# Performance work log

Measured on AMD Instinct MI355X. Metric: run time of the kernel, lower is better.

The kernel has to match this reference:

```python
import jax, jax.numpy as jnp
import numpy as np

N = 50000       # nodes
E = 1200000     # edges (before self-loops)
IN_CH = 128
HID = 64
L = 3           # FAConv layers
EPS_RES = 0.1   # FAConv eps residual weight
BN_EPS = 1e-5


def _bn(x, g, b):
    # BatchNorm1d, training-mode statistics (biased variance, like torch)
    mu = x.mean(axis=0)
    var = x.var(axis=0)
    return g * (x - mu) * jax.lax.rsqrt(var + BN_EPS) + b


def setup_inputs() -> dict:
    key = jax.random.key(0)
    ks = jax.random.split(key, 12)
    s = lambda d: 1.0 / np.sqrt(d)
    H2 = HID // 2
    return {
        "x": jax.random.normal(ks[0], (N, IN_CH), jnp.float32),
        "edge_index": jax.random.randint(ks[1], (2, E), 0, N, dtype=jnp.int32),
        "batch_size": 10000,
        "W_in": jax.random.normal(ks[2], (IN_CH, HID), jnp.float32) * s(IN_CH),
        "b_in": jnp.zeros((HID,), jnp.float32),
        "att_l": jax.random.normal(ks[3], (L, HID), jnp.float32) * s(HID),
        "att_r": jax.random.normal(ks[4], (L, HID), jnp.float32) * s(HID),
        "bn_g": jnp.ones((L, HID), jnp.float32),
        "bn_b": jnp.zeros((L, HID), jnp.float32),
        "W1": jax.random.normal(ks[5], (HID, HID), jnp.float32) * s(HID),
        "b1": jnp.zeros((HID,), jnp.float32),
        "g1": jnp.ones((HID,), jnp.float32),
        "be1": jnp.zeros((HID,), jnp.float32),
        "W2": jax.random.normal(ks[6], (HID, H2), jnp.float32) * s(HID),
        "b2": jnp.zeros((H2,), jnp.float32),
        "g2": jnp.ones((H2,), jnp.float32),
        "be2": jnp.zeros((H2,), jnp.float32),
        "W3": jax.random.normal(ks[7], (H2, 1), jnp.float32) * s(H2),
        "b3": jnp.zeros((1,), jnp.float32),
    }


def reference(x, edge_index, batch_size, W_in, b_in, att_l, att_r, bn_g, bn_b,
              W1, b1, g1, be1, W2, b2, g2, be2, W3, b3):
    n = x.shape[0]
    # gcn_norm with self-loops (same for all layers since graph is fixed)
    loops = jnp.arange(n, dtype=edge_index.dtype)
    src = jnp.concatenate([edge_index[0], loops])  # j (source)
    dst = jnp.concatenate([edge_index[1], loops])  # i (target)
    deg = jax.ops.segment_sum(jnp.ones_like(dst, dtype=x.dtype), dst, num_segments=n)
    dinv = jnp.where(deg > 0, jax.lax.rsqrt(deg), 0.0)
    norm = dinv[src] * dinv[dst]                   # [E+N]

    x0 = jax.nn.relu(x @ W_in + b_in)              # [N, HID]
    h = x0
    for l in range(L):
        al = h @ att_l[l]                          # [N] att_l^T x
        ar = h @ att_r[l]                          # [N] att_r^T x
        alpha = jnp.tanh(al[src] + ar[dst])        # [E+N] signed attention
        msg = h[src] * (alpha * norm)[:, None]     # gather + weight
        out = jax.ops.segment_sum(msg, dst, num_segments=n) + EPS_RES * x0
        h = _bn(jax.nn.relu(out), bn_g[l], bn_b[l])

    z = h[:batch_size]
    z = jax.nn.relu(_bn(z @ W1 + b1, g1, be1))
    z = jax.nn.relu(_bn(z @ W2 + b2, g2, be2))
    return (z @ W3 + b3).squeeze(-1)
```

## Files before the change

kernel.cpp:

```cpp
#include <hip/hip_runtime.h>
#include <hip/hip_bf16.h>
#include <math.h>

#define NND 50000
#define NE  1200000
#define TOT (NE + NND)
#define INCH 128
#define HID 64
#define H2  32
#define NL  3
#define BSZ 10000
#define NB  196
#define NHB 128
#define NSTAT 256
#define CHUNK 4096
#define EPS_RES 0.1f
#define BN_EPS 1e-5f

typedef unsigned short ushort8v __attribute__((ext_vector_type(8)));

__device__ __forceinline__ float b2f(unsigned short u) {
    return __uint_as_float((unsigned)u << 16);
}

__device__ __forceinline__ float fast_tanh(float x) {
    float cx = fminf(fmaxf(x, -8.f), 8.f);
    float e = __expf(2.f * cx);
    return 1.f - __fdividef(2.f, e + 1.f);
}


__global__ __launch_bounds__(256) void bhist_kernel(const int* __restrict__ dst, int* __restrict__ bh_part, int ne) {
    __shared__ int arr[256];
    arr[threadIdx.x] = 0;
    __syncthreads();
    int i = blockIdx.x * 256 + threadIdx.x;
    int stride = gridDim.x * 256;
    for (int e = i; e < ne; e += stride) atomicAdd(&arr[dst[e] >> 8], 1);
    __syncthreads();
    bh_part[blockIdx.x * 256 + threadIdx.x] = arr[threadIdx.x];
}

__global__ __launch_bounds__(256) void bscan_kernel(const int* __restrict__ bh_part,
                                                    int* __restrict__ bstart, int* __restrict__ bcur,
                                                    int* __restrict__ offsets) {
    __shared__ int ls[256];
    int t = threadIdx.x;
    int v = 0;
    for (int k = 0; k < NHB; k++) v += bh_part[k * 256 + t];
    ls[t] = v;
    __syncthreads();
    for (int off = 1; off < 256; off <<= 1) {
        int tv = (t >= off) ? ls[t - off] : 0;
        __syncthreads();
        ls[t] += tv;
        __syncthreads();
    }
    int excl = ls[t] - v;
    if (t < NB) { bstart[t] = excl; bcur[t] = excl; }
    if (t == NB) bstart[NB] = ls[NB - 1];
    if (t == 0) offsets[NND] = TOT;
}

__global__ __launch_bounds__(256) void passA_kernel(const int* __restrict__ src, const int* __restrict__ dst,
                                                    int* __restrict__ bcur, unsigned* __restrict__ ebuf, int ne) {
    __shared__ int arr[256];
    int t = threadIdx.x;
    int base = blockIdx.x * CHUNK;
    int lim = min(base + CHUNK, ne);
    arr[t] = 0;
    __syncthreads();
    for (int e = base + t; e < lim; e += 256) atomicAdd(&arr[dst[e] >> 8], 1);
    __syncthreads();
    int cnt_t = arr[t];
    int claimed = 0;
    if (cnt_t > 0) claimed = atomicAdd(&bcur[t], cnt_t);
    __syncthreads();
    arr[t] = claimed;
    __syncthreads();
    for (int e = base + t; e < lim; e += 256) {
        int d = dst[e];
        int pos = atomicAdd(&arr[d >> 8], 1);
        ebuf[pos] = ((unsigned)src[e] << 8) | (unsigned)(d & 255);
    }
}

__global__ __launch_bounds__(256) void bucket_build_kernel(const unsigned* __restrict__ ebuf, const int* __restrict__ bstart,
                                                           int* __restrict__ offsets, int* __restrict__ csr,
                                                           float* __restrict__ aldi_f) {
    __shared__ int dcnt[256];
    __shared__ int ls[256];
    __shared__ int cur[256];
    int b = blockIdx.x, t = threadIdx.x;
    dcnt[t] = 0;
    __syncthreads();
    int beg = bstart[b], end = bstart[b + 1];
    for (int p = beg + t; p < end; p += 256) atomicAdd(&dcnt[ebuf[p] & 255u], 1);
    __syncthreads();
    int node = b * 256 + t;
    bool valid = node < NND;
    int d = valid ? (dcnt[t] + 1) : 0;
    ls[t] = d;
    __syncthreads();
    for (int off = 1; off < 256; off <<= 1) {
        int tv = (t >= off) ? ls[t - off] : 0;
        __syncthreads();
        ls[t] += tv;
        __syncthreads();
    }
    int off = bstart[b] + b * 256 + ls[t] - d;
    if (valid) {
        offsets[node] = off;
        aldi_f[2 * node + 1] = rsqrtf((float)d);
        csr[off] = node;
        cur[t] = off + 1;
    }
    __syncthreads();
    for (int p = beg + t; p < end; p += 256) {
        unsigned ed = ebuf[p];
        int pos = atomicAdd(&cur[ed & 255u], 1);
        csr[pos] = (int)(ed >> 8);
    }
}

__global__ __launch_bounds__(256) void gemm_in_kernel(const float* __restrict__ x, const float* __restrict__ W,
                                                      const float* __restrict__ b,
                                                      const float* __restrict__ attl, const float* __restrict__ attr,
                                                      __hip_bfloat16* __restrict__ x0bf,
                                                      float* __restrict__ aldi_f, float* __restrict__ ar) {
    __shared__ float Wl[INCH * HID];
    __shared__ float xs[16 * INCH];
    int t = threadIdx.x;
    for (int i = t; i < INCH * HID; i += 256) Wl[i] = W[i];
    size_t rowbase = (size_t)blockIdx.x * 16;
    for (int i = t; i < 16 * INCH; i += 256) xs[i] = x[rowbase * INCH + i];
    __syncthreads();
    int col = t & 63, rg = t >> 6;
    float a0 = 0.f, a1 = 0.f, a2 = 0.f, a3 = 0.f;
    for (int k = 0; k < INCH; k++) {
        float wk = Wl[k * HID + col];
        a0 = fmaf(xs[(rg * 4 + 0) * INCH + k], wk, a0);
        a1 = fmaf(xs[(rg * 4 + 1) * INCH + k], wk, a1);
        a2 = fmaf(xs[(rg * 4 + 2) * INCH + k], wk, a2);
        a3 = fmaf(xs[(rg * 4 + 3) * INCH + k], wk, a3);
    }
    float bb = b[col];
    a0 = fmaxf(a0 + bb, 0.f); a1 = fmaxf(a1 + bb, 0.f);
    a2 = fmaxf(a2 + bb, 0.f); a3 = fmaxf(a3 + bb, 0.f);
    size_t r = rowbase + rg * 4;
    x0bf[(r + 0) * HID + col] = __float2bfloat16(a0);
    x0bf[(r + 1) * HID + col] = __float2bfloat16(a1);
    x0bf[(r + 2) * HID + col] = __float2bfloat16(a2);
    x0bf[(r + 3) * HID + col] = __float2bfloat16(a3);
    float wl = attl[col], wr = attr[col];
    float p0 = a0 * wl, q0 = a0 * wr, p1 = a1 * wl, q1 = a1 * wr;
    float p2 = a2 * wl, q2 = a2 * wr, p3 = a3 * wl, q3 = a3 * wr;
    for (int off = 32; off > 0; off >>= 1) {
        p0 += __shfl_xor(p0, off); q0 += __shfl_xor(q0, off);
        p1 += __shfl_xor(p1, off); q1 += __shfl_xor(q1, off);
        p2 += __shfl_xor(p2, off); q2 += __shfl_xor(q2, off);
        p3 += __shfl_xor(p3, off); q3 += __shfl_xor(q3, off);
    }
    if (col == 0) {
        aldi_f[2 * (r + 0)] = p0; ar[r + 0] = q0;
        aldi_f[2 * (r + 1)] = p1; ar[r + 1] = q1;
        aldi_f[2 * (r + 2)] = p2; ar[r + 2] = q2;
        aldi_f[2 * (r + 3)] = p3; ar[r + 3] = q3;
    }
}

__global__ __launch_bounds__(256) void aggregate_kernel(const __hip_bfloat16* __restrict__ hbf,
                                                        const __hip_bfloat16* __restrict__ x0bf,
                                                        const float2* __restrict__ aldi,
                                                        const float* __restrict__ ar,
                                                        const int* __restrict__ offsets, const int* __restrict__ csr,
                                                        float* __restrict__ y, int n) {
    int v = (blockIdx.x * 256 + threadIdx.x) >> 6;
    int lane = threadIdx.x & 63;
    if (v >= n) return;
    int g = lane >> 3;
    int cl = (lane & 7) << 3;
    int beg = offsets[v], end = offsets[v + 1];
    float arv = ar[v];
    const unsigned short* hb = (const unsigned short*)hbf;
    float a0 = 0.f, a1 = 0.f, a2 = 0.f, a3 = 0.f, a4 = 0.f, a5 = 0.f, a6 = 0.f, a7 = 0.f;
    for (int base = beg; base < end; base += 64) {
        int p = base + lane;
        int u = 0; float c = 0.f;
        if (p < end) {
            u = csr[p];
            float2 ad = aldi[u];
            c = fast_tanh(ad.x + arv) * ad.y;
        }
        int cnt = min(64, end - base);
        int iters = (cnt + 7) >> 3;
        int j = g;
        int js = (j < cnt) ? j : 0;
        int uj = __shfl(u, js);
        float cj = __shfl(c, js);
        if (j >= cnt) cj = 0.f;
        ushort8v hv = *(const ushort8v*)(hb + (size_t)uj * HID + cl);
        for (int it = 1; it < iters; ++it) {
            int jn = (it << 3) + g;
            int jsn = (jn < cnt) ? jn : 0;
            int ujn = __shfl(u, jsn);
            float cjn = __shfl(c, jsn);
            if (jn >= cnt) cjn = 0.f;
            ushort8v hvn = *(const ushort8v*)(hb + (size_t)ujn * HID + cl);
            a0 = fmaf(b2f(hv[0]), cj, a0);
            a1 = fmaf(b2f(hv[1]), cj, a1);
            a2 = fmaf(b2f(hv[2]), cj, a2);
            a3 = fmaf(b2f(hv[3]), cj, a3);
            a4 = fmaf(b2f(hv[4]), cj, a4);
            a5 = fmaf(b2f(hv[5]), cj, a5);
            a6 = fmaf(b2f(hv[6]), cj, a6);
            a7 = fmaf(b2f(hv[7]), cj, a7);
            hv = hvn; cj = cjn;
        }
        a0 = fmaf(b2f(hv[0]), cj, a0);
        a1 = fmaf(b2f(hv[1]), cj, a1);
        a2 = fmaf(b2f(hv[2]), cj, a2);
        a3 = fmaf(b2f(hv[3]), cj, a3);
        a4 = fmaf(b2f(hv[4]), cj, a4);
        a5 = fmaf(b2f(hv[5]), cj, a5);
        a6 = fmaf(b2f(hv[6]), cj, a6);
        a7 = fmaf(b2f(hv[7]), cj, a7);
    }
    for (int off = 8; off < 64; off <<= 1) {
        a0 += __shfl_xor(a0, off); a1 += __shfl_xor(a1, off);
        a2 += __shfl_xor(a2, off); a3 += __shfl_xor(a3, off);
        a4 += __shfl_xor(a4, off); a5 += __shfl_xor(a5, off);
        a6 += __shfl_xor(a6, off); a7 += __shfl_xor(a7, off);
    }
    if (g == 0) {
        float dv = aldi[v].y;
        ushort8v xb = *(const ushort8v*)((const unsigned short*)x0bf + (size_t)v * HID + cl);
        float4 o0, o1;
        o0.x = fmaxf(fmaf(EPS_RES, b2f(xb[0]), a0 * dv), 0.f);
        o0.y = fmaxf(fmaf(EPS_RES, b2f(xb[1]), a1 * dv), 0.f);
        o0.z = fmaxf(fmaf(EPS_RES, b2f(xb[2]), a2 * dv), 0.f);
        o0.w = fmaxf(fmaf(EPS_RES, b2f(xb[3]), a3 * dv), 0.f);
        o1.x = fmaxf(fmaf(EPS_RES, b2f(xb[4]), a4 * dv), 0.f);
        o1.y = fmaxf(fmaf(EPS_RES, b2f(xb[5]), a5 * dv), 0.f);
        o1.z = fmaxf(fmaf(EPS_RES, b2f(xb[6]), a6 * dv), 0.f);
        o1.w = fmaxf(fmaf(EPS_RES, b2f(xb[7]), a7 * dv), 0.f);
        *(float4*)(y + (size_t)v * HID + cl) = o0;
        *(float4*)(y + (size_t)v * HID + cl + 4) = o1;
    }
}

template <int C>
__global__ __launch_bounds__(256) void bn_stats_fused_kernel(const float* __restrict__ y, int rows,
                                                             const float* __restrict__ g, const float* __restrict__ b,
                                                             float rows_inv,
                                                             float* __restrict__ acc, int* __restrict__ counter,
                                                             float* __restrict__ scale, float* __restrict__ shift) {
    const int TPR = C / 4;
    const int RPW = 64 / TPR;
    int lane = threadIdx.x & 63;
    int wave = threadIdx.x >> 6;
    int cl = (lane % TPR) * 4;
    int rsub = lane / TPR;
    int rpb = 4 * RPW;
    int r = blockIdx.x * rpb + wave * RPW + rsub;
    int stride = gridDim.x * rpb;
    float s0 = 0.f, s1 = 0.f, s2 = 0.f, s3 = 0.f, q0 = 0.f, q1 = 0.f, q2 = 0.f, q3 = 0.f;
    for (; r < rows; r += stride) {
        float4 v = *(const float4*)(y + (size_t)r * C + cl);
        s0 += v.x; q0 = fmaf(v.x, v.x, q0);
        s1 += v.y; q1 = fmaf(v.y, v.y, q1);
        s2 += v.z; q2 = fmaf(v.z, v.z, q2);
        s3 += v.w; q3 = fmaf(v.w, v.w, q3);
    }
    for (int off = TPR; off < 64; off <<= 1) {
        s0 += __shfl_xor(s0, off); q0 += __shfl_xor(q0, off);
        s1 += __shfl_xor(s1, off); q1 += __shfl_xor(q1, off);
        s2 += __shfl_xor(s2, off); q2 += __shfl_xor(q2, off);
        s3 += __shfl_xor(s3, off); q3 += __shfl_xor(q3, off);
    }
    __shared__ float lsum[4][64], lsq[4][64];
    if (lane < TPR) {
        lsum[wave][cl + 0] = s0; lsq[wave][cl + 0] = q0;
        lsum[wave][cl + 1] = s1; lsq[wave][cl + 1] = q1;
        lsum[wave][cl + 2] = s2; lsq[wave][cl + 2] = q2;
        lsum[wave][cl + 3] = s3; lsq[wave][cl + 3] = q3;
    }
    __syncthreads();
    int t = threadIdx.x;
    if (t < C) {
        float ts = lsum[0][t] + lsum[1][t] + lsum[2][t] + lsum[3][t];
        float tq = lsq[0][t] + lsq[1][t] + lsq[2][t] + lsq[3][t];
        atomicAdd(&acc[t], ts);
        atomicAdd(&acc[64 + t], tq);
    }
    __shared__ int islast;
    __syncthreads();
    if (t == 0) {
        __threadfence();
        int old = atomicAdd(counter, 1);
        islast = (old == (int)gridDim.x - 1) ? 1 : 0;
    }
    __syncthreads();
    if (islast && t < C) {
        float ts = atomicAdd(&acc[t], 0.f);
        float tq = atomicAdd(&acc[64 + t], 0.f);
        float mean = ts * rows_inv;
        float var = tq * rows_inv - mean * mean;
        float sc = g[t] * rsqrtf(var + BN_EPS);
        scale[t] = sc;
        shift[t] = b[t] - mean * sc;
        atomicExch(&acc[t], 0.f);
        atomicExch(&acc[64 + t], 0.f);
        if (t == 0) atomicExch(counter, 0);
    }
}

__global__ __launch_bounds__(256) void bnapply_attn_kernel(const float* __restrict__ y, const float* __restrict__ scale,
                                                           const float* __restrict__ shift,
                                                           const float* __restrict__ attl, const float* __restrict__ attr,
                                                           __hip_bfloat16* __restrict__ hbf,
                                                           float* __restrict__ aldi_f, float* __restrict__ ar, int n) {
    int v = (blockIdx.x * 256 + threadIdx.x) >> 6;
    int lane = threadIdx.x & 63;
    if (v >= n) return;
    float val = fmaf(y[(size_t)v * HID + lane], scale[lane], shift[lane]);
    hbf[(size_t)v * HID + lane] = __float2bfloat16(val);
    float pl = val * attl[lane];
    float pr = val * attr[lane];
    for (int off = 32; off > 0; off >>= 1) {
        pl += __shfl_xor(pl, off);
        pr += __shfl_xor(pr, off);
    }
    if (lane == 0) { aldi_f[2 * v] = pl; ar[v] = pr; }
}

__global__ __launch_bounds__(256) void mlp1_kernel(const float* __restrict__ y, const float* __restrict__ scale,
                                                   const float* __restrict__ shift, const float* __restrict__ W,
                                                   const float* __restrict__ b, float* __restrict__ z1) {
    __shared__ float Wl[HID * HID];
    __shared__ float xs[16 * HID];
    int t = threadIdx.x;
    for (int i = t; i < HID * HID; i += 256) Wl[i] = W[i];
    size_t rowbase = (size_t)blockIdx.x * 16;
    for (int i = t; i < 16 * HID; i += 256) {
        int c = i & 63;
        xs[i] = fmaf(y[rowbase * HID + i], scale[c], shift[c]);
    }
    __syncthreads();
    int col = t & 63, rg = t >> 6;
    float a0 = 0.f, a1 = 0.f, a2 = 0.f, a3 = 0.f;
    for (int k = 0; k < HID; k++) {
        float wk = Wl[k * HID + col];
        a0 = fmaf(xs[(rg * 4 + 0) * HID + k], wk, a0);
        a1 = fmaf(xs[(rg * 4 + 1) * HID + k], wk, a1);
        a2 = fmaf(xs[(rg * 4 + 2) * HID + k], wk, a2);
        a3 = fmaf(xs[(rg * 4 + 3) * HID + k], wk, a3);
    }
    float bb = b[col];
    size_t r = rowbase + rg * 4;
    z1[(r + 0) * HID + col] = a0 + bb;
    z1[(r + 1) * HID + col] = a1 + bb;
    z1[(r + 2) * HID + col] = a2 + bb;
    z1[(r + 3) * HID + col] = a3 + bb;
}

__global__ __launch_bounds__(256) void mlp2_kernel(const float* __restrict__ z1, const float* __restrict__ scale,
                                                   const float* __restrict__ shift, const float* __restrict__ W,
                                                   const float* __restrict__ b, float* __restrict__ z2) {
    __shared__ float Wl[HID * H2];
    __shared__ float as[16 * HID];
    int t = threadIdx.x;
    for (int i = t; i < HID * H2; i += 256) Wl[i] = W[i];
    size_t rowbase = (size_t)blockIdx.x * 16;
    for (int i = t; i < 16 * HID; i += 256) {
        int c = i & 63;
        float v = z1[rowbase * HID + i];
        as[i] = fmaxf(fmaf(v, scale[c], shift[c]), 0.f);
    }
    __syncthreads();
    int col = t & 31, rg = t >> 5;
    float a0 = 0.f, a1 = 0.f;
    for (int k = 0; k < HID; k++) {
        float wk = Wl[k * H2 + col];
        a0 = fmaf(as[(rg * 2 + 0) * HID + k], wk, a0);
        a1 = fmaf(as[(rg * 2 + 1) * HID + k], wk, a1);
    }
    float bb = b[col];
    size_t r = rowbase + rg * 2;
    z2[(r + 0) * H2 + col] = a0 + bb;
    z2[(r + 1) * H2 + col] = a1 + bb;
}

__global__ __launch_bounds__(256) void mlp3_kernel(const float* __restrict__ z2, const float* __restrict__ scale,
                                                   const float* __restrict__ shift, const float* __restrict__ W3,
                                                   const float* __restrict__ b3, float* __restrict__ out, int rows) {
    int i = blockIdx.x * 256 + threadIdx.x;
    if (i >= rows) return;
    float acc = 0.f;
#pragma unroll
    for (int k = 0; k < H2; k++) {
        float v = fmaxf(fmaf(z2[(size_t)i * H2 + k], scale[k], shift[k]), 0.f);
        acc = fmaf(v, W3[k], acc);
    }
    out[i] = acc + b3[0];
}

extern "C" void kernel_launch(void* const* d_in, const int* in_sizes, int n_in,
                              void* d_out, int out_size, void* d_ws, size_t ws_size,
                              hipStream_t stream) {
    const float* x     = (const float*)d_in[0];
    const int*   ei    = (const int*)d_in[1];
    const int*   src   = ei;
    const int*   dst   = ei + NE;
    const float* W_in  = (const float*)d_in[3];
    const float* b_in  = (const float*)d_in[4];
    const float* att_l = (const float*)d_in[5];
    const float* att_r = (const float*)d_in[6];
    const float* bn_g  = (const float*)d_in[7];
    const float* bn_b  = (const float*)d_in[8];
    const float* W1    = (const float*)d_in[9];
    const float* b1    = (const float*)d_in[10];
    const float* g1    = (const float*)d_in[11];
    const float* be1   = (const float*)d_in[12];
    const float* W2    = (const float*)d_in[13];
    const float* b2    = (const float*)d_in[14];
    const float* g2    = (const float*)d_in[15];
    const float* be2   = (const float*)d_in[16];
    const float* W3    = (const float*)d_in[17];
    const float* b3    = (const float*)d_in[18];
    float* out = (float*)d_out;

    char* p = (char*)d_ws;
    auto carve = [&](size_t bytes) -> void* {
        void* r = (void*)p;
        p += (bytes + 255) & ~(size_t)255;
        return r;
    };
    int*   bh_part = (int*)carve((size_t)NHB * 256 * 4);
    int*   bstart  = (int*)carve(256 * 4);
    int*   bcur    = (int*)carve(256 * 4);
    int*   offsets = (int*)carve((size_t)(NND + 1) * 4);
    int*   csr     = (int*)carve((size_t)TOT * 4);
    float2* aldi   = (float2*)carve((size_t)NND * 8);
    float* ar      = (float*)carve((size_t)NND * 4);
    __hip_bfloat16* x0bf = (__hip_bfloat16*)carve((size_t)NND * HID * 2);
    __hip_bfloat16* hbfA = (__hip_bfloat16*)carve((size_t)NND * HID * 2);
    __hip_bfloat16* hbfB = (__hip_bfloat16*)carve((size_t)NND * HID * 2);
    float* ybuf    = (float*)carve((size_t)NND * HID * 4);
    unsigned* ebuf = (unsigned*)ybuf;
    float* acc     = (float*)carve(132 * 4);
    int*   counter = (int*)(acc + 128);
    float* scale   = (float*)carve(64 * 4);
    float* shift   = (float*)carve(64 * 4);
    float* z1      = (float*)carve((size_t)BSZ * HID * 4);
    float* z2      = (float*)carve((size_t)BSZ * H2 * 4);

    const int nblkA = (NE + CHUNK - 1) / CHUNK;

    hipMemsetAsync(acc, 0, 132 * 4, stream);

    bhist_kernel<<<NHB, 256, 0, stream>>>(dst, bh_part, NE);
    gemm_in_kernel<<<NND / 16, 256, 0, stream>>>(x, W_in, b_in, att_l, att_r, x0bf, (float*)aldi, ar);
    bscan_kernel<<<1, 256, 0, stream>>>(bh_part, bstart, bcur, offsets);
    passA_kernel<<<nblkA, 256, 0, stream>>>(src, dst, bcur, ebuf, NE);
    bucket_build_kernel<<<NB, 256, 0, stream>>>(ebuf, bstart, offsets, csr, (float*)aldi);

    const __hip_bfloat16* h_in = x0bf;
    __hip_bfloat16* hbufs[2] = {hbfA, hbfB};
    for (int l = 0; l < NL; l++) {
        aggregate_kernel<<<NND / 4, 256, 0, stream>>>(h_in, x0bf, aldi, ar, offsets, csr, ybuf, NND);
        bn_stats_fused_kernel<64><<<NSTAT, 256, 0, stream>>>(ybuf, NND, bn_g + l * HID, bn_b + l * HID,
                                                             1.0f / NND, acc, counter, scale, shift);
        if (l < NL - 1) {
            bnapply_attn_kernel<<<NND / 4, 256, 0, stream>>>(ybuf, scale, shift,
                                                             att_l + (l + 1) * HID, att_r + (l + 1) * HID,
                                                             hbufs[l], (float*)aldi, ar, NND);
            h_in = hbufs[l];
        }
    }

    mlp1_kernel<<<BSZ / 16, 256, 0, stream>>>(ybuf, scale, shift, W1, b1, z1);
    bn_stats_fused_kernel<64><<<NSTAT, 256, 0, stream>>>(z1, BSZ, g1, be1, 1.0f / BSZ, acc, counter, scale, shift);

    mlp2_kernel<<<BSZ / 16, 256, 0, stream>>>(z1, scale, shift, W2, b2, z2);
    bn_stats_fused_kernel<32><<<NSTAT, 256, 0, stream>>>(z2, BSZ, g2, be2, 1.0f / BSZ, acc, counter, scale, shift);

    mlp3_kernel<<<(BSZ + 255) / 256, 256, 0, stream>>>(z2, scale, shift, W3, b3, out, BSZ);
}
```

Measured before the change: 364.5 us.

## Fuse BN stats with apply via grid barrier; unroll aggregate gather by four

Merges the BatchNorm statistics kernel and the BN-apply/attention kernel for the first two layers into one persistent kernel that spins on a global counter as a grid-wide barrier. This saves a launch and keeps part of the feature buffer warm in cache. The aggregate loop is also restructured to issue four independent neighbour row loads per iteration instead of a one-deep software prefetch, to get more memory parallelism. Each BN use now gets its own zeroed accumulator slot instead of resetting shared ones, which relies on all 256 blocks being co-resident for the spin barrier.

```diff
diff --git a/kernel.cpp b/kernel.cpp
--- a/kernel.cpp
+++ b/kernel.cpp
@@ -193,38 +193,39 @@
             c = fast_tanh(ad.x + arv) * ad.y;
         }
         int cnt = min(64, end - base);
-        int iters = (cnt + 7) >> 3;
-        int j = g;
-        int js = (j < cnt) ? j : 0;
-        int uj = __shfl(u, js);
-        float cj = __shfl(c, js);
-        if (j >= cnt) cj = 0.f;
-        ushort8v hv = *(const ushort8v*)(hb + (size_t)uj * HID + cl);
-        for (int it = 1; it < iters; ++it) {
-            int jn = (it << 3) + g;
-            int jsn = (jn < cnt) ? jn : 0;
-            int ujn = __shfl(u, jsn);
-            float cjn = __shfl(c, jsn);
-            if (jn >= cnt) cjn = 0.f;
-            ushort8v hvn = *(const ushort8v*)(hb + (size_t)ujn * HID + cl);
-            a0 = fmaf(b2f(hv[0]), cj, a0);
-            a1 = fmaf(b2f(hv[1]), cj, a1);
-            a2 = fmaf(b2f(hv[2]), cj, a2);
-            a3 = fmaf(b2f(hv[3]), cj, a3);
-            a4 = fmaf(b2f(hv[4]), cj, a4);
-            a5 = fmaf(b2f(hv[5]), cj, a5);
-            a6 = fmaf(b2f(hv[6]), cj, a6);
-            a7 = fmaf(b2f(hv[7]), cj, a7);
-            hv = hvn; cj = cjn;
+        int nchunk = (cnt + 31) >> 5;
+        for (int ch = 0; ch < nchunk; ++ch) {
+            int j0 = (ch << 5) + g;
+            int j1 = j0 + 8, j2 = j0 + 16, j3 = j0 + 24;
+            int js0 = (j0 < cnt) ? j0 : 0;
+            int js1 = (j1 < cnt) ? j1 : 0;
+            int js2 = (j2 < cnt) ? j2 : 0;
+            int js3 = (j3 < cnt) ? j3 : 0;
+            int u0 = __shfl(u, js0); float c0 = __shfl(c, js0); if (j0 >= cnt) c0 = 0.f;
+            int u1 = __shfl(u, js1); float c1 = __shfl(c, js1); if (j1 >= cnt) c1 = 0.f;
+            int u2 = __shfl(u, js2); float c2 = __shfl(c, js2); if (j2 >= cnt) c2 = 0.f;
+            int u3 = __shfl(u, js3); float c3 = __shfl(c, js3); if (j3 >= cnt) c3 = 0.f;
+            ushort8v h0 = *(const ushort8v*)(hb + (size_t)u0 * HID + cl);
+            ushort8v h1 = *(const ushort8v*)(hb + (size_t)u1 * HID + cl);
+            ushort8v h2 = *(const ushort8v*)(hb + (size_t)u2 * HID + cl);
+            ushort8v h3 = *(const ushort8v*)(hb + (size_t)u3 * HID + cl);
+            a0 = fmaf(b2f(h0[0]), c0, a0); a1 = fmaf(b2f(h0[1]), c0, a1);
+            a2 = fmaf(b2f(h0[2]), c0, a2); a3 = fmaf(b2f(h0[3]), c0, a3);
+            a4 = fmaf(b2f(h0[4]), c0, a4); a5 = fmaf(b2f(h0[5]), c0, a5);
+            a6 = fmaf(b2f(h0[6]), c0, a6); a7 = fmaf(b2f(h0[7]), c0, a7);
+            a0 = fmaf(b2f(h1[0]), c1, a0); a1 = fmaf(b2f(h1[1]), c1, a1);
+            a2 = fmaf(b2f(h1[2]), c1, a2); a3 = fmaf(b2f(h1[3]), c1, a3);
+            a4 = fmaf(b2f(h1[4]), c1, a4); a5 = fmaf(b2f(h1[5]), c1, a5);
+            a6 = fmaf(b2f(h1[6]), c1, a6); a7 = fmaf(b2f(h1[7]), c1, a7);
+            a0 = fmaf(b2f(h2[0]), c2, a0); a1 = fmaf(b2f(h2[1]), c2, a1);
+            a2 = fmaf(b2f(h2[2]), c2, a2); a3 = fmaf(b2f(h2[3]), c2, a3);
+            a4 = fmaf(b2f(h2[4]), c2, a4); a5 = fmaf(b2f(h2[5]), c2, a5);
+            a6 = fmaf(b2f(h2[6]), c2, a6); a7 = fmaf(b2f(h2[7]), c2, a7);
+            a0 = fmaf(b2f(h3[0]), c3, a0); a1 = fmaf(b2f(h3[1]), c3, a1);
+            a2 = fmaf(b2f(h3[2]), c3, a2); a3 = fmaf(b2f(h3[3]), c3, a3);
+            a4 = fmaf(b2f(h3[4]), c3, a4); a5 = fmaf(b2f(h3[5]), c3, a5);
+            a6 = fmaf(b2f(h3[6]), c3, a6); a7 = fmaf(b2f(h3[7]), c3, a7);
         }
-        a0 = fmaf(b2f(hv[0]), cj, a0);
-        a1 = fmaf(b2f(hv[1]), cj, a1);
-        a2 = fmaf(b2f(hv[2]), cj, a2);
-        a3 = fmaf(b2f(hv[3]), cj, a3);
-        a4 = fmaf(b2f(hv[4]), cj, a4);
-        a5 = fmaf(b2f(hv[5]), cj, a5);
-        a6 = fmaf(b2f(hv[6]), cj, a6);
-        a7 = fmaf(b2f(hv[7]), cj, a7);
     }
     for (int off = 8; off < 64; off <<= 1) {
         a0 += __shfl_xor(a0, off); a1 += __shfl_xor(a1, off);
@@ -309,29 +310,90 @@
         float sc = g[t] * rsqrtf(var + BN_EPS);
         scale[t] = sc;
         shift[t] = b[t] - mean * sc;
-        atomicExch(&acc[t], 0.f);
-        atomicExch(&acc[64 + t], 0.f);
-        if (t == 0) atomicExch(counter, 0);
-    }
-}
-
-__global__ __launch_bounds__(256) void bnapply_attn_kernel(const float* __restrict__ y, const float* __restrict__ scale,
-                                                           const float* __restrict__ shift,
-                                                           const float* __restrict__ attl, const float* __restrict__ attr,
-                                                           __hip_bfloat16* __restrict__ hbf,
-                                                           float* __restrict__ aldi_f, float* __restrict__ ar, int n) {
-    int v = (blockIdx.x * 256 + threadIdx.x) >> 6;
+    }
+}
+
+__global__ __launch_bounds__(256) void bn_fused_apply_attn_kernel(const float* __restrict__ y, int rows,
+                                                                  const float* __restrict__ g, const float* __restrict__ b,
+                                                                  float rows_inv,
+                                                                  float* __restrict__ acc, int* __restrict__ counter,
+                                                                  const float* __restrict__ attl, const float* __restrict__ attr,
+                                                                  __hip_bfloat16* __restrict__ hbf,
+                                                                  float* __restrict__ aldi_f, float* __restrict__ ar) {
+    const int TPR = 16;
     int lane = threadIdx.x & 63;
-    if (v >= n) return;
-    float val = fmaf(y[(size_t)v * HID + lane], scale[lane], shift[lane]);
-    hbf[(size_t)v * HID + lane] = __float2bfloat16(val);
-    float pl = val * attl[lane];
-    float pr = val * attr[lane];
-    for (int off = 32; off > 0; off >>= 1) {
-        pl += __shfl_xor(pl, off);
-        pr += __shfl_xor(pr, off);
-    }
-    if (lane == 0) { aldi_f[2 * v] = pl; ar[v] = pr; }
+    int wave = threadIdx.x >> 6;
+    int cl = (lane % TPR) * 4;
+    int rsub = lane / TPR;
+    int r = blockIdx.x * 16 + wave * 4 + rsub;
+    int stride = gridDim.x * 16;
+    float s0 = 0.f, s1 = 0.f, s2 = 0.f, s3 = 0.f, q0 = 0.f, q1 = 0.f, q2 = 0.f, q3 = 0.f;
+    for (; r < rows; r += stride) {
+        float4 v = *(const float4*)(y + (size_t)r * HID + cl);
+        s0 += v.x; q0 = fmaf(v.x, v.x, q0);
+        s1 += v.y; q1 = fmaf(v.y, v.y, q1);
+        s2 += v.z; q2 = fmaf(v.z, v.z, q2);
+        s3 += v.w; q3 = fmaf(v.w, v.w, q3);
+    }
+    for (int off = TPR; off < 64; off <<= 1) {
+        s0 += __shfl_xor(s0, off); q0 += __shfl_xor(q0, off);
+        s1 += __shfl_xor(s1, off); q1 += __shfl_xor(q1, off);
+        s2 += __shfl_xor(s2, off); q2 += __shfl_xor(q2, off);
+        s3 += __shfl_xor(s3, off); q3 += __shfl_xor(q3, off);
+    }
+    __shared__ float lsum[4][64], lsq[4][64];
+    if (lane < TPR) {
+        lsum[wave][cl + 0] = s0; lsq[wave][cl + 0] = q0;
+        lsum[wave][cl + 1] = s1; lsq[wave][cl + 1] = q1;
+        lsum[wave][cl + 2] = s2; lsq[wave][cl + 2] = q2;
+        lsum[wave][cl + 3] = s3; lsq[wave][cl + 3] = q3;
+    }
+    __syncthreads();
+    int t = threadIdx.x;
+    if (t < 64) {
+        float ts = lsum[0][t] + lsum[1][t] + lsum[2][t] + lsum[3][t];
+        float tq = lsq[0][t] + lsq[1][t] + lsq[2][t] + lsq[3][t];
+        atomicAdd(&acc[t], ts);
+        atomicAdd(&acc[64 + t], tq);
+    }
+    __syncthreads();
+    if (t == 0) {
+        __threadfence();
+        atomicAdd(counter, 1);
+        while (atomicAdd(counter, 0) < (int)gridDim.x) {
+            __builtin_amdgcn_s_sleep(2);
+        }
+    }
+    __syncthreads();
+    __shared__ float s_scale[64], s_shift[64];
+    if (t < 64) {
+        float ts = atomicAdd(&acc[t], 0.f);
+        float tq = atomicAdd(&acc[64 + t], 0.f);
+        float mean = ts * rows_inv;
+        float var = tq * rows_inv - mean * mean;
+        float sc = g[t] * rsqrtf(var + BN_EPS);
+        s_scale[t] = sc;
+        s_shift[t] = b[t] - mean * sc;
+    }
+    __syncthreads();
+    float scl = s_scale[lane], shf = s_shift[lane];
+    float wl = attl[lane], wr = attr[lane];
+    for (int r0 = blockIdx.x * 16 + wave * 4; r0 < rows; r0 += stride) {
+#pragma unroll
+        for (int i = 0; i < 4; i++) {
+            int rr = r0 + i;
+            if (rr >= rows) break;
+            float val = fmaf(y[(size_t)rr * HID + lane], scl, shf);
+            hbf[(size_t)rr * HID + lane] = __float2bfloat16(val);
+            float pl = val * wl;
+            float pr = val * wr;
+            for (int off = 32; off > 0; off >>= 1) {
+                pl += __shfl_xor(pl, off);
+                pr += __shfl_xor(pr, off);
+            }
+            if (lane == 0) { aldi_f[2 * rr] = pl; ar[rr] = pr; }
+        }
+    }
 }
 
 __global__ __launch_bounds__(256) void mlp1_kernel(const float* __restrict__ y, const float* __restrict__ scale,
@@ -448,16 +510,18 @@
     __hip_bfloat16* hbfB = (__hip_bfloat16*)carve((size_t)NND * HID * 2);
     float* ybuf    = (float*)carve((size_t)NND * HID * 4);
     unsigned* ebuf = (unsigned*)ybuf;
-    float* acc     = (float*)carve(132 * 4);
-    int*   counter = (int*)(acc + 128);
+    float* accall  = (float*)carve(5 * 256 * 4);
     float* scale   = (float*)carve(64 * 4);
     float* shift   = (float*)carve(64 * 4);
     float* z1      = (float*)carve((size_t)BSZ * HID * 4);
     float* z2      = (float*)carve((size_t)BSZ * H2 * 4);
 
+    auto accr = [&](int i) -> float* { return accall + i * 256; };
+    auto ctr  = [&](int i) -> int*   { return (int*)(accall + i * 256 + 128); };
+
     const int nblkA = (NE + CHUNK - 1) / CHUNK;
 
-    hipMemsetAsync(acc, 0, 132 * 4, stream);
+    hipMemsetAsync(accall, 0, 5 * 256 * 4, stream);
 
     bhist_kernel<<<NHB, 256, 0, stream>>>(dst, bh_part, NE);
     gemm_in_kernel<<<NND / 16, 256, 0, stream>>>(x, W_in, b_in, att_l, att_r, x0bf, (float*)aldi, ar);
@@ -469,21 +533,23 @@
     __hip_bfloat16* hbufs[2] = {hbfA, hbfB};
     for (int l = 0; l < NL; l++) {
         aggregate_kernel<<<NND / 4, 256, 0, stream>>>(h_in, x0bf, aldi, ar, offsets, csr, ybuf, NND);
-        bn_stats_fused_kernel<64><<<NSTAT, 256, 0, stream>>>(ybuf, NND, bn_g + l * HID, bn_b + l * HID,
-                                                             1.0f / NND, acc, counter, scale, shift);
         if (l < NL - 1) {
-            bnapply_attn_kernel<<<NND / 4, 256, 0, stream>>>(ybuf, scale, shift,
-                                                             att_l + (l + 1) * HID, att_r + (l + 1) * HID,
-                                                             hbufs[l], (float*)aldi, ar, NND);
+            bn_fused_apply_attn_kernel<<<NSTAT, 256, 0, stream>>>(ybuf, NND, bn_g + l * HID, bn_b + l * HID,
+                                                                  1.0f / NND, accr(l), ctr(l),
+                                                                  att_l + (l + 1) * HID, att_r + (l + 1) * HID,
+                                                                  hbufs[l], (float*)aldi, ar);
             h_in = hbufs[l];
+        } else {
+            bn_stats_fused_kernel<64><<<NSTAT, 256, 0, stream>>>(ybuf, NND, bn_g + l * HID, bn_b + l * HID,
+                                                                 1.0f / NND, accr(2), ctr(2), scale, shift);
         }
     }
 
     mlp1_kernel<<<BSZ / 16, 256, 0, stream>>>(ybuf, scale, shift, W1, b1, z1);
-    bn_stats_fused_kernel<64><<<NSTAT, 256, 0, stream>>>(z1, BSZ, g1, be1, 1.0f / BSZ, acc, counter, scale, shift);
+    bn_stats_fused_kernel<64><<<NSTAT, 256, 0, stream>>>(z1, BSZ, g1, be1, 1.0f / BSZ, accr(3), ctr(3), scale, shift);
 
     mlp2_kernel<<<BSZ / 16, 256, 0, stream>>>(z1, scale, shift, W2, b2, z2);
-    bn_stats_fused_kernel<32><<<NSTAT, 256, 0, stream>>>(z2, BSZ, g2, be2, 1.0f / BSZ, acc, counter, scale, shift);
+    bn_stats_fused_kernel<32><<<NSTAT, 256, 0, stream>>>(z2, BSZ, g2, be2, 1.0f / BSZ, accr(4), ctr(4), scale, shift);
 
     mlp3_kernel<<<(BSZ + 255) / 256, 256, 0, stream>>>(z2, scale, shift, W3, b3, out, BSZ);
 }
```

New measurement: 396.6 us. 1.09x slower.
